# Kernel tuning notes

Hardware: AMD Instinct MI355X
Metric: run time of the kernel (lower is better)

## Reference

```python
import jax, jax.numpy as jnp
import numpy as np

T, B, D_IN, D_LAT, D_OUT = 2048, 64, 256, 256, 256


def _linear_params(key, fan_in, fan_out):
    kw, kb = jax.random.split(key)
    bound = 1.0 / np.sqrt(fan_in)
    W = jax.random.uniform(kw, (fan_out, fan_in), jnp.float32, -bound, bound)
    b = jax.random.uniform(kb, (fan_out,), jnp.float32, -bound, bound)
    return W, b


def setup_inputs() -> dict:
    key = jax.random.key(0)
    ks = jax.random.split(key, 6)
    Wf, bf = _linear_params(ks[0], D_IN + D_LAT, D_LAT)
    Wi, bi = _linear_params(ks[1], D_IN + D_LAT, D_LAT)
    Wo, bo = _linear_params(ks[2], D_IN + D_LAT, D_LAT)
    Wc, bc = _linear_params(ks[3], D_IN + D_LAT, D_LAT)
    Wout, bout = _linear_params(ks[4], D_LAT, D_OUT)
    x = jax.random.normal(ks[5], (T, B, D_IN), jnp.float32)
    h0 = jnp.zeros((B, D_LAT), jnp.float32)
    C0 = jnp.zeros((B, D_LAT), jnp.float32)
    return {"x": x, "h0": h0, "C0": C0,
            "Wf": Wf, "bf": bf, "Wi": Wi, "bi": bi,
            "Wo": Wo, "bo": bo, "Wc": Wc, "bc": bc,
            "Wout": Wout, "bout": bout}


def reference(x, h0, C0, Wf, bf, Wi, bi, Wo, bo, Wc, bc, Wout, bout):
    def step(carry, x_t):
        h, C = carry
        comb = jnp.concatenate([x_t, h], axis=-1)  # [B, D_IN+D_LAT]
        f_t = jax.nn.sigmoid(comb @ Wf.T + bf)
        i_t = jax.nn.sigmoid(comb @ Wi.T + bi)
        o_t = jax.nn.sigmoid(comb @ Wo.T + bo)
        C_tilde = jnp.tanh(comb @ Wc.T + bc)
        C_new = f_t * C + i_t * C_tilde
        h_new = o_t * jnp.tanh(C_new)
        out = h_new @ Wout.T + bout
        return (h_new, C_new), (out, h_new)
    (h_f, C_f), (outputs, hidden_states) = jax.lax.scan(step, (h0, C0), x)
    return outputs, hidden_states, C_f
```

## Files before the change

### kernel.cpp

```cpp
#include <hip/hip_runtime.h>
#include <cstdint>
#include <cstddef>

#define T_STEPS 2048
#define BATCH 64

typedef _Float16 f16;
typedef _Float16 f16x2 __attribute__((ext_vector_type(2)));
typedef _Float16 f16x8 __attribute__((ext_vector_type(8)));
typedef float f32x4 __attribute__((ext_vector_type(4)));
typedef unsigned int uint32;
typedef unsigned long long uint64;
typedef uint32 u32x4 __attribute__((ext_vector_type(4)));

__device__ __forceinline__ float dot2(uint32 w, uint32 h, float c) {
  f16x2 a = __builtin_bit_cast(f16x2, w);
  f16x2 b = __builtin_bit_cast(f16x2, h);
  return __builtin_amdgcn_fdot2(a, b, c, false);
}

__device__ __forceinline__ float dot8(u32x4 w, u32x4 h, float c) {
  c = dot2(w[0], h[0], c);
  c = dot2(w[1], h[1], c);
  c = dot2(w[2], h[2], c);
  c = dot2(w[3], h[3], c);
  return c;
}

__device__ __forceinline__ uint32 pack2(f16 a, f16 b) {
  f16x2 t; t[0] = a; t[1] = b;
  return __builtin_bit_cast(uint32, t);
}

__global__ __launch_bounds__(256) void setup_weights(
    const float* __restrict__ Wf, const float* __restrict__ Wi,
    const float* __restrict__ Wo, const float* __restrict__ Wc,
    const float* __restrict__ Wout,
    f16* __restrict__ wx16, f16* __restrict__ wout16, uint32* __restrict__ whp)
{
  int id = blockIdx.x * 256 + threadIdx.x;
  const float* WG_[4] = {Wf, Wi, Wo, Wc};
  if (id < 262144) {
    int n = id >> 8, k = id & 255;
    int G = n >> 8, j = n & 255;
    wx16[id] = (f16)WG_[G][j * 512 + k];
    return;
  }
  id -= 262144;
  if (id < 65536) { wout16[id] = (f16)Wout[id]; return; }
  id -= 65536;
  if (id < 131072) {
    int kq = id >> 12, rem = id & 4095;
    int o = rem >> 2, c = rem & 3;
    int G = o >> 8, j = o & 255;
    const float* src = WG_[G] + j * 512 + 256 + kq * 8 + c * 2;
    whp[id] = pack2((f16)src[0], (f16)src[1]);
  }
}

__global__ __launch_bounds__(256) void setup_state(
    const float* __restrict__ h0, const float* __restrict__ C0,
    uint64* __restrict__ hpair, float* __restrict__ c32)
{
  int id = blockIdx.x * 256 + threadIdx.x;
  if (id < 8192) {
    int slot = id >> 6, i = id & 63;
    int r = slot >> 1, hf = slot & 1;
    const float* hr = h0 + r * 256 + hf * 128 + 2 * i;
    uint32 a = (uint32)__builtin_bit_cast(unsigned short, (f16)hr[0]);
    uint32 b = (uint32)__builtin_bit_cast(unsigned short, (f16)hr[1]);
    hpair[id] = ((uint64)b << 32) | (uint64)a;
    return;
  }
  id -= 8192;
  if (id < 8192) { hpair[8192 + id] = 0xFFFF0000FFFF0000ULL; return; }
  id -= 8192;
  if (id < 16384) c32[id] = C0[id];
}

template<int A_F32, int OUT_F32_BIAS>
__global__ __launch_bounds__(256) void gemm_k(
    const void* __restrict__ Av, const f16* __restrict__ B,
    void* __restrict__ Cv, const float* __restrict__ bias, int N)
{
  constexpr int LDA = 264;
  __shared__ f16 As[128 * 264];
  __shared__ f16 Bs[128 * 264];
  const int tid = threadIdx.x;
  const int m0 = blockIdx.x * 128;
  const int n0 = blockIdx.y * 128;

  if (A_F32) {
    const float* A = (const float*)Av;
    #pragma unroll
    for (int j = 0; j < 32; ++j) {
      int flat = (tid + j * 256) * 4;
      int row = flat >> 8, col = flat & 255;
      const float4 v = *(const float4*)(A + (size_t)(m0 + row) * 256 + col);
      uint2 u; u.x = pack2((f16)v.x, (f16)v.y); u.y = pack2((f16)v.z, (f16)v.w);
      *(uint2*)&As[row * LDA + col] = u;
    }
  } else {
    const f16* A = (const f16*)Av;
    #pragma unroll
    for (int j = 0; j < 32; ++j) {
      int flat = (tid + j * 256) * 4;
      int row = flat >> 8, col = flat & 255;
      *(uint2*)&As[row * LDA + col] = *(const uint2*)(A + (size_t)(m0 + row) * 256 + col);
    }
  }
  #pragma unroll
  for (int j = 0; j < 32; ++j) {
    int flat = (tid + j * 256) * 4;
    int row = flat >> 8, col = flat & 255;
    *(uint2*)&Bs[row * LDA + col] = *(const uint2*)(B + (size_t)(n0 + row) * 256 + col);
  }
  __syncthreads();

  const int wave = tid >> 6, l = tid & 63;
  const int wr = wave >> 1, wc = wave & 1;
  const int lr = l & 15, lq = l >> 4;

  f32x4 acc[4][4] = {};
  #pragma unroll
  for (int kk = 0; kk < 8; ++kk) {
    f16x8 a[4], b[4];
    #pragma unroll
    for (int mi = 0; mi < 4; ++mi)
      a[mi] = *(const f16x8*)&As[(64 * wr + 16 * mi + lr) * LDA + kk * 32 + lq * 8];
    #pragma unroll
    for (int ni = 0; ni < 4; ++ni)
      b[ni] = *(const f16x8*)&Bs[(64 * wc + 16 * ni + lr) * LDA + kk * 32 + lq * 8];
    #pragma unroll
    for (int mi = 0; mi < 4; ++mi)
      #pragma unroll
      for (int ni = 0; ni < 4; ++ni)
        acc[mi][ni] = __builtin_amdgcn_mfma_f32_16x16x32_f16(a[mi], b[ni], acc[mi][ni], 0, 0, 0);
  }

  #pragma unroll
  for (int mi = 0; mi < 4; ++mi) {
    #pragma unroll
    for (int ni = 0; ni < 4; ++ni) {
      int col = n0 + 64 * wc + 16 * ni + lr;
      float bv = 0.f;
      if (OUT_F32_BIAS) bv = bias[col];
      #pragma unroll
      for (int v = 0; v < 4; ++v) {
        int row = m0 + 64 * wr + 16 * mi + lq * 4 + v;
        if (OUT_F32_BIAS) ((float*)Cv)[(size_t)row * N + col] = acc[mi][ni][v] + bv;
        else              ((f16*)Cv)[(size_t)row * N + col] = (f16)acc[mi][ni][v];
      }
    }
  }
}

#define RLO16(M) M(0) M(1) M(2) M(3) M(4) M(5) M(6) M(7) M(8) M(9) M(10) M(11) \
  M(12) M(13) M(14) M(15)
#define RLS4(M) M(0) M(1) M(2) M(3)

__global__ __launch_bounds__(512) void lstm_persist(
    const uint32* __restrict__ whp,
    const float* __restrict__ bf, const float* __restrict__ bi,
    const float* __restrict__ bo, const float* __restrict__ bc,
    const f16* __restrict__ xproj, uint64* __restrict__ hpair,
    float* __restrict__ c32, float* __restrict__ hid_out,
    f16* __restrict__ h16c, float* __restrict__ cf_out, int t0, int Tc)
{
  __shared__ u32x4 wlds[12 * 512];
  __shared__ uint32 h_lds[128] __attribute__((aligned(16)));
  __shared__ float part[4 * 132];
  __shared__ unsigned short hstage[128];

  const int tid = threadIdx.x;
  const int w = blockIdx.x;
  const int hf  = (w >> 3) & 1;
  const int r   = (w & 7) | ((w >> 4) << 3);
  const int G = tid >> 7, jjl = tid & 127;
  const int j = hf * 128 + jjl;
  const int o = (G << 8) + j;

  const int hfo = hf * 64;
  const int sfo = (hf ^ 1) * 64;
  const int okq = hf * 16;
  const int skq = (hf ^ 1) * 16;

  const u32x4* wq = (const u32x4*)whp;

#define LOADO(i) u32x4 wo##i = wq[(okq + (i)) * 1024 + o];
  RLO16(LOADO)
#undef LOADO
#define LOADS(i) u32x4 ws##i = wq[(skq + (i)) * 1024 + o];
  RLS4(LOADS)
#undef LOADS
  #pragma unroll
  for (int i = 0; i < 12; ++i)
    wlds[i * 512 + tid] = wq[(skq + 4 + i) * 1024 + o];

  const float* bGp = (G == 0) ? bf : (G == 1) ? bi : (G == 2) ? bo : bc;
  const float biasv = bGp[j];

  float Creg = 0.f;
  if (tid < 128) Creg = c32[r * 256 + j];

  uint64* mybuf  = hpair + (size_t)(r * 2 + hf) * 64;
  uint64* sibbuf = hpair + (size_t)(r * 2 + (hf ^ 1)) * 64;

  for (int tl = 0; tl < Tc; ++tl) {
    const int gt = t0 + tl;
    const int pp = gt & 1;

    const float xpv = (float)xproj[((size_t)tl * 64 + r) * 1024 + o];

    if (tid < 64) {
      const uint64* p = sibbuf + (size_t)pp * 8192 + tid;
      const uint32 tg = (uint32)gt;
      uint64 v = __hip_atomic_load(p, __ATOMIC_RELAXED, __HIP_MEMORY_SCOPE_AGENT);
      int tries = 0;
      while (((((uint32)v) >> 16) != tg || ((uint32)(v >> 48)) != tg) &&
             ++tries < (1 << 22)) {
        v = __hip_atomic_load(p, __ATOMIC_RELAXED, __HIP_MEMORY_SCOPE_AGENT);
      }
      h_lds[sfo + tid] =
          (((uint32)v) & 0xFFFFu) | ((((uint32)(v >> 32)) & 0xFFFFu) << 16);
    } else if (tl == 0 && tid < 128) {
      const int i = tid - 64;
      const uint64* p = mybuf + (size_t)pp * 8192 + i;
      const uint32 tg = (uint32)gt;
      uint64 v = __hip_atomic_load(p, __ATOMIC_RELAXED, __HIP_MEMORY_SCOPE_AGENT);
      int tries = 0;
      while (((((uint32)v) >> 16) != tg || ((uint32)(v >> 48)) != tg) &&
             ++tries < (1 << 22)) {
        v = __hip_atomic_load(p, __ATOMIC_RELAXED, __HIP_MEMORY_SCOPE_AGENT);
      }
      h_lds[hfo + i] =
          (((uint32)v) & 0xFFFFu) | ((((uint32)(v >> 32)) & 0xFFFFu) << 16);
    }
    __syncthreads();

    int otid;
    asm volatile("v_mov_b32 %0, %1" : "=v"(otid) : "v"(tid));
    float acc = 0.f;
#define DOT_O(i) { const u32x4 hh = *(const u32x4*)&h_lds[hfo + (i) * 4]; \
                   acc = dot8(wo##i, hh, acc); }
    RLO16(DOT_O)
#undef DOT_O
#define DOT_S(i) { const u32x4 hh = *(const u32x4*)&h_lds[sfo + (i) * 4]; \
                   acc = dot8(ws##i, hh, acc); }
    RLS4(DOT_S)
#undef DOT_S
    #pragma unroll
    for (int i = 0; i < 12; ++i) {
      const u32x4 hh = *(const u32x4*)&h_lds[sfo + (4 + i) * 4];
      acc = dot8(wlds[i * 512 + otid], hh, acc);
    }
    part[G * 132 + jjl] = acc + xpv + biasv;
    __syncthreads();

    if (tid < 128) {
      const float pf = part[tid];
      const float pi = part[132 + tid];
      const float po = part[264 + tid];
      const float pc = part[396 + tid];
      const float f_ = __builtin_amdgcn_rcpf(1.f + __expf(-pf));
      const float i_ = __builtin_amdgcn_rcpf(1.f + __expf(-pi));
      const float o_ = __builtin_amdgcn_rcpf(1.f + __expf(-po));
      const float cb = 1.f - 2.f * __builtin_amdgcn_rcpf(__expf(2.f * pc) + 1.f);
      const float Cn = f_ * Creg + i_ * cb;
      Creg = Cn;
      const float th = 1.f - 2.f * __builtin_amdgcn_rcpf(__expf(2.f * Cn) + 1.f);
      const float hn = o_ * th;
      hid_out[((size_t)gt * 64 + r) * 256 + j] = hn;
      const f16 h16v = (f16)hn;
      hstage[tid] = __builtin_bit_cast(unsigned short, h16v);
      h16c[((size_t)tl * 64 + r) * 256 + j] = h16v;
      if (gt == T_STEPS - 1) cf_out[r * 256 + j] = Cn;
    }
    __syncthreads();

    if (tid < 64) {
      const uint32 a = (uint32)hstage[2 * tid];
      const uint32 b = (uint32)hstage[2 * tid + 1];
      h_lds[hfo + tid] = a | (b << 16);
      const uint32 tg1u = ((uint32)(gt + 1)) << 16;
      const uint64 v = ((uint64)(b | tg1u) << 32) | (uint64)(a | tg1u);
      __hip_atomic_store(mybuf + (size_t)((gt + 1) & 1) * 8192 + tid, v,
                         __ATOMIC_RELAXED, __HIP_MEMORY_SCOPE_AGENT);
    }
  }

  if (tid < 128) c32[r * 256 + j] = Creg;
}

extern "C" void kernel_launch(void* const* d_in, const int* in_sizes, int n_in,
                              void* d_out, int out_size, void* d_ws, size_t ws_size,
                              hipStream_t stream)
{
  const float* x    = (const float*)d_in[0];
  const float* h0   = (const float*)d_in[1];
  const float* C0   = (const float*)d_in[2];
  const float* Wf   = (const float*)d_in[3];
  const float* bf   = (const float*)d_in[4];
  const float* Wi   = (const float*)d_in[5];
  const float* bi   = (const float*)d_in[6];
  const float* Wo   = (const float*)d_in[7];
  const float* bo   = (const float*)d_in[8];
  const float* Wc   = (const float*)d_in[9];
  const float* bc   = (const float*)d_in[10];
  const float* Wout = (const float*)d_in[11];
  const float* bout = (const float*)d_in[12];
  float* out = (float*)d_out;

  char* w = (char*)d_ws;
  f16*    wx16   = (f16*)w;    w += (size_t)1024 * 256 * 2;
  f16*    wout16 = (f16*)w;    w += (size_t)256 * 256 * 2;
  uint32* whp    = (uint32*)w; w += (size_t)131072 * 4;
  uint64* hpair  = (uint64*)w; w += (size_t)2 * 8192 * 8;
  float*  c32    = (float*)w;  w += (size_t)64 * 256 * 4;
  const size_t fixedB = (size_t)(w - (char*)d_ws);

  int Tc = 2;
  const int cands[] = {2048, 1024, 512, 256, 128, 64, 32, 16, 8, 4, 2};
  for (int c : cands) {
    if (fixedB + (size_t)c * 163840 <= ws_size) { Tc = c; break; }
  }

  f16* xproj = (f16*)w;
  f16* h16c  = (f16*)(w + (size_t)Tc * 64 * 1024 * 2);

  setup_weights<<<1792, 256, 0, stream>>>(Wf, Wi, Wo, Wc, Wout,
                                          wx16, wout16, whp);
  setup_state<<<128, 256, 0, stream>>>(h0, C0, hpair, c32);

  float* hid_out = out + (size_t)T_STEPS * 64 * 256;
  float* cf_out  = out + (size_t)2 * T_STEPS * 64 * 256;

  for (int t0 = 0; t0 < T_STEPS; t0 += Tc) {
    gemm_k<1, 0><<<dim3(Tc * 64 / 128, 8), 256, 0, stream>>>(
        x + (size_t)t0 * 64 * 256, wx16, xproj, nullptr, 1024);
    lstm_persist<<<128, 512, 0, stream>>>(whp, bf, bi, bo, bc,
                                          xproj, hpair, c32,
                                          hid_out, h16c, cf_out, t0, Tc);
    gemm_k<0, 1><<<dim3(Tc * 64 / 128, 2), 256, 0, stream>>>(
        h16c, wout16, out + (size_t)t0 * 64 * 256, bout, 256);
  }
}
```

Measured before the change: 3.711 ms.

## Split each batch row's LSTM hidden units across four workgroups instead of two

New measurement: 3.813 ms. 1.03x slower.

```diff
diff --git a/kernel.cpp b/kernel.cpp
--- a/kernel.cpp
+++ b/kernel.cpp
@@ -60,20 +60,20 @@
 
 __global__ __launch_bounds__(256) void setup_state(
     const float* __restrict__ h0, const float* __restrict__ C0,
-    uint64* __restrict__ hpair, float* __restrict__ c32)
+    uint64* __restrict__ hbuf, float* __restrict__ c32)
 {
   int id = blockIdx.x * 256 + threadIdx.x;
   if (id < 8192) {
-    int slot = id >> 6, i = id & 63;
-    int r = slot >> 1, hf = slot & 1;
-    const float* hr = h0 + r * 256 + hf * 128 + 2 * i;
+    int slot = id >> 5, i = id & 31;
+    int r = slot >> 2, q = slot & 3;
+    const float* hr = h0 + r * 256 + q * 64 + 2 * i;
     uint32 a = (uint32)__builtin_bit_cast(unsigned short, (f16)hr[0]);
     uint32 b = (uint32)__builtin_bit_cast(unsigned short, (f16)hr[1]);
-    hpair[id] = ((uint64)b << 32) | (uint64)a;
+    hbuf[id] = ((uint64)b << 32) | (uint64)a;
     return;
   }
   id -= 8192;
-  if (id < 8192) { hpair[8192 + id] = 0xFFFF0000FFFF0000ULL; return; }
+  if (id < 8192) { hbuf[8192 + id] = 0xFFFF0000FFFF0000ULL; return; }
   id -= 8192;
   if (id < 16384) c32[id] = C0[id];
 }
@@ -155,56 +155,45 @@
   }
 }
 
-#define RLO16(M) M(0) M(1) M(2) M(3) M(4) M(5) M(6) M(7) M(8) M(9) M(10) M(11) \
-  M(12) M(13) M(14) M(15)
-#define RLS4(M) M(0) M(1) M(2) M(3)
-
-__global__ __launch_bounds__(512) void lstm_persist(
+#define RL20(M) M(0) M(1) M(2) M(3) M(4) M(5) M(6) M(7) M(8) M(9) M(10) M(11) \
+  M(12) M(13) M(14) M(15) M(16) M(17) M(18) M(19)
+
+__global__ __launch_bounds__(256) void lstm_persist(
     const uint32* __restrict__ whp,
     const float* __restrict__ bf, const float* __restrict__ bi,
     const float* __restrict__ bo, const float* __restrict__ bc,
-    const f16* __restrict__ xproj, uint64* __restrict__ hpair,
+    const f16* __restrict__ xproj, uint64* __restrict__ hbuf,
     float* __restrict__ c32, float* __restrict__ hid_out,
     f16* __restrict__ h16c, float* __restrict__ cf_out, int t0, int Tc)
 {
-  __shared__ u32x4 wlds[12 * 512];
+  __shared__ u32x4 wlds[12 * 256];
   __shared__ uint32 h_lds[128] __attribute__((aligned(16)));
-  __shared__ float part[4 * 132];
-  __shared__ unsigned short hstage[128];
+  __shared__ float part[4 * 68];
+  __shared__ unsigned short hstage[64];
 
   const int tid = threadIdx.x;
   const int w = blockIdx.x;
-  const int hf  = (w >> 3) & 1;
-  const int r   = (w & 7) | ((w >> 4) << 3);
-  const int G = tid >> 7, jjl = tid & 127;
-  const int j = hf * 128 + jjl;
+  const int q = w >> 6, r = w & 63;
+  const int G = tid >> 6, col = tid & 63;
+  const int j = q * 64 + col;
   const int o = (G << 8) + j;
 
-  const int hfo = hf * 64;
-  const int sfo = (hf ^ 1) * 64;
-  const int okq = hf * 16;
-  const int skq = (hf ^ 1) * 16;
-
   const u32x4* wq = (const u32x4*)whp;
 
-#define LOADO(i) u32x4 wo##i = wq[(okq + (i)) * 1024 + o];
-  RLO16(LOADO)
-#undef LOADO
-#define LOADS(i) u32x4 ws##i = wq[(skq + (i)) * 1024 + o];
-  RLS4(LOADS)
-#undef LOADS
+#define LOADW(i) u32x4 w##i = wq[(i) * 1024 + o];
+  RL20(LOADW)
+#undef LOADW
   #pragma unroll
   for (int i = 0; i < 12; ++i)
-    wlds[i * 512 + tid] = wq[(skq + 4 + i) * 1024 + o];
+    wlds[i * 256 + tid] = wq[(20 + i) * 1024 + o];
 
   const float* bGp = (G == 0) ? bf : (G == 1) ? bi : (G == 2) ? bo : bc;
   const float biasv = bGp[j];
 
   float Creg = 0.f;
-  if (tid < 128) Creg = c32[r * 256 + j];
-
-  uint64* mybuf  = hpair + (size_t)(r * 2 + hf) * 64;
-  uint64* sibbuf = hpair + (size_t)(r * 2 + (hf ^ 1)) * 64;
+  if (tid < 64) Creg = c32[r * 256 + q * 64 + tid];
+
+  uint64* mybuf = hbuf + (size_t)(r * 4 + q) * 32;
 
   for (int tl = 0; tl < Tc; ++tl) {
     const int gt = t0 + tl;
@@ -212,56 +201,54 @@
 
     const float xpv = (float)xproj[((size_t)tl * 64 + r) * 1024 + o];
 
-    if (tid < 64) {
-      const uint64* p = sibbuf + (size_t)pp * 8192 + tid;
+    if (tid < 96) {
+      const int s = tid >> 5, i = tid & 31;
+      const int qq = s + (s >= q ? 1 : 0);
+      const uint64* p = hbuf + (size_t)pp * 8192 + (size_t)(r * 4 + qq) * 32 + i;
       const uint32 tg = (uint32)gt;
       uint64 v = __hip_atomic_load(p, __ATOMIC_RELAXED, __HIP_MEMORY_SCOPE_AGENT);
       int tries = 0;
       while (((((uint32)v) >> 16) != tg || ((uint32)(v >> 48)) != tg) &&
-             ++tries < (1 << 22)) {
+             ++tries < (1 << 20)) {
         v = __hip_atomic_load(p, __ATOMIC_RELAXED, __HIP_MEMORY_SCOPE_AGENT);
       }
-      h_lds[sfo + tid] =
+      h_lds[qq * 32 + i] =
           (((uint32)v) & 0xFFFFu) | ((((uint32)(v >> 32)) & 0xFFFFu) << 16);
     } else if (tl == 0 && tid < 128) {
-      const int i = tid - 64;
+      const int i = tid - 96;
       const uint64* p = mybuf + (size_t)pp * 8192 + i;
       const uint32 tg = (uint32)gt;
       uint64 v = __hip_atomic_load(p, __ATOMIC_RELAXED, __HIP_MEMORY_SCOPE_AGENT);
       int tries = 0;
       while (((((uint32)v) >> 16) != tg || ((uint32)(v >> 48)) != tg) &&
-             ++tries < (1 << 22)) {
+             ++tries < (1 << 20)) {
         v = __hip_atomic_load(p, __ATOMIC_RELAXED, __HIP_MEMORY_SCOPE_AGENT);
       }
-      h_lds[hfo + i] =
+      h_lds[q * 32 + i] =
           (((uint32)v) & 0xFFFFu) | ((((uint32)(v >> 32)) & 0xFFFFu) << 16);
     }
     __syncthreads();
 
     int otid;
     asm volatile("v_mov_b32 %0, %1" : "=v"(otid) : "v"(tid));
-    float acc = 0.f;
-#define DOT_O(i) { const u32x4 hh = *(const u32x4*)&h_lds[hfo + (i) * 4]; \
-                   acc = dot8(wo##i, hh, acc); }
-    RLO16(DOT_O)
-#undef DOT_O
-#define DOT_S(i) { const u32x4 hh = *(const u32x4*)&h_lds[sfo + (i) * 4]; \
-                   acc = dot8(ws##i, hh, acc); }
-    RLS4(DOT_S)
-#undef DOT_S
+    float ac[4] = {0.f, 0.f, 0.f, 0.f};
+#define DOTW(i) { const u32x4 hh = *(const u32x4*)&h_lds[(i) * 4]; \
+                  ac[(i) & 3] = dot8(w##i, hh, ac[(i) & 3]); }
+    RL20(DOTW)
+#undef DOTW
     #pragma unroll
     for (int i = 0; i < 12; ++i) {
-      const u32x4 hh = *(const u32x4*)&h_lds[sfo + (4 + i) * 4];
-      acc = dot8(wlds[i * 512 + otid], hh, acc);
-    }
-    part[G * 132 + jjl] = acc + xpv + biasv;
+      const u32x4 hh = *(const u32x4*)&h_lds[(20 + i) * 4];
+      ac[(20 + i) & 3] = dot8(wlds[i * 256 + otid], hh, ac[(20 + i) & 3]);
+    }
+    part[G * 68 + col] = (ac[0] + ac[1]) + (ac[2] + ac[3]) + xpv + biasv;
     __syncthreads();
 
-    if (tid < 128) {
+    if (tid < 64) {
       const float pf = part[tid];
-      const float pi = part[132 + tid];
-      const float po = part[264 + tid];
-      const float pc = part[396 + tid];
+      const float pi = part[68 + tid];
+      const float po = part[136 + tid];
+      const float pc = part[204 + tid];
       const float f_ = __builtin_amdgcn_rcpf(1.f + __expf(-pf));
       const float i_ = __builtin_amdgcn_rcpf(1.f + __expf(-pi));
       const float o_ = __builtin_amdgcn_rcpf(1.f + __expf(-po));
@@ -270,18 +257,19 @@
       Creg = Cn;
       const float th = 1.f - 2.f * __builtin_amdgcn_rcpf(__expf(2.f * Cn) + 1.f);
       const float hn = o_ * th;
-      hid_out[((size_t)gt * 64 + r) * 256 + j] = hn;
+      const int jg = q * 64 + tid;
+      hid_out[((size_t)gt * 64 + r) * 256 + jg] = hn;
       const f16 h16v = (f16)hn;
       hstage[tid] = __builtin_bit_cast(unsigned short, h16v);
-      h16c[((size_t)tl * 64 + r) * 256 + j] = h16v;
-      if (gt == T_STEPS - 1) cf_out[r * 256 + j] = Cn;
+      h16c[((size_t)tl * 64 + r) * 256 + jg] = h16v;
+      if (gt == T_STEPS - 1) cf_out[r * 256 + jg] = Cn;
     }
     __syncthreads();
 
-    if (tid < 64) {
+    if (tid < 32) {
       const uint32 a = (uint32)hstage[2 * tid];
       const uint32 b = (uint32)hstage[2 * tid + 1];
-      h_lds[hfo + tid] = a | (b << 16);
+      h_lds[q * 32 + tid] = a | (b << 16);
       const uint32 tg1u = ((uint32)(gt + 1)) << 16;
       const uint64 v = ((uint64)(b | tg1u) << 32) | (uint64)(a | tg1u);
       __hip_atomic_store(mybuf + (size_t)((gt + 1) & 1) * 8192 + tid, v,
@@ -289,7 +277,7 @@
     }
   }
 
-  if (tid < 128) c32[r * 256 + j] = Creg;
+  if (tid < 64) c32[r * 256 + q * 64 + tid] = Creg;
 }
 
 extern "C" void kernel_launch(void* const* d_in, const int* in_sizes, int n_in,
@@ -315,7 +303,7 @@
   f16*    wx16   = (f16*)w;    w += (size_t)1024 * 256 * 2;
   f16*    wout16 = (f16*)w;    w += (size_t)256 * 256 * 2;
   uint32* whp    = (uint32*)w; w += (size_t)131072 * 4;
-  uint64* hpair  = (uint64*)w; w += (size_t)2 * 8192 * 8;
+  uint64* hbuf   = (uint64*)w; w += (size_t)2 * 8192 * 8;
   float*  c32    = (float*)w;  w += (size_t)64 * 256 * 4;
   const size_t fixedB = (size_t)(w - (char*)d_ws);
 
@@ -330,7 +318,7 @@
 
   setup_weights<<<1792, 256, 0, stream>>>(Wf, Wi, Wo, Wc, Wout,
                                           wx16, wout16, whp);
-  setup_state<<<128, 256, 0, stream>>>(h0, C0, hpair, c32);
+  setup_state<<<128, 256, 0, stream>>>(h0, C0, hbuf, c32);
 
   float* hid_out = out + (size_t)T_STEPS * 64 * 256;
   float* cf_out  = out + (size_t)2 * T_STEPS * 64 * 256;
@@ -338,8 +326,8 @@
   for (int t0 = 0; t0 < T_STEPS; t0 += Tc) {
     gemm_k<1, 0><<<dim3(Tc * 64 / 128, 8), 256, 0, stream>>>(
         x + (size_t)t0 * 64 * 256, wx16, xproj, nullptr, 1024);
-    lstm_persist<<<128, 512, 0, stream>>>(whp, bf, bi, bo, bc,
-                                          xproj, hpair, c32,
+    lstm_persist<<<256, 256, 0, stream>>>(whp, bf, bi, bo, bc,
+                                          xproj, hbuf, c32,
                                           hid_out, h16c, cf_out, t0, Tc);
     gemm_k<0, 1><<<dim3(Tc * 64 / 128, 2), 256, 0, stream>>>(
         h16c, wout16, out + (size_t)t0 * 64 * 256, bout, 256);
```

## Gather LSTM gates with wave shuffles and overlap own-half dot with sibling wait

Applied to the files above, without the earlier changes.

Measured after the change: 3.376 ms. 1.1x faster.

```diff
diff --git a/kernel.cpp b/kernel.cpp
--- a/kernel.cpp
+++ b/kernel.cpp
@@ -60,7 +60,7 @@
 
 __global__ __launch_bounds__(256) void setup_state(
     const float* __restrict__ h0, const float* __restrict__ C0,
-    uint64* __restrict__ hpair, float* __restrict__ c32)
+    uint64* __restrict__ hbuf, float* __restrict__ c32)
 {
   int id = blockIdx.x * 256 + threadIdx.x;
   if (id < 8192) {
@@ -69,11 +69,11 @@
     const float* hr = h0 + r * 256 + hf * 128 + 2 * i;
     uint32 a = (uint32)__builtin_bit_cast(unsigned short, (f16)hr[0]);
     uint32 b = (uint32)__builtin_bit_cast(unsigned short, (f16)hr[1]);
-    hpair[id] = ((uint64)b << 32) | (uint64)a;
+    hbuf[id] = ((uint64)b << 32) | (uint64)a;
     return;
   }
   id -= 8192;
-  if (id < 8192) { hpair[8192 + id] = 0xFFFF0000FFFF0000ULL; return; }
+  if (id < 8192) { hbuf[8192 + id] = 0xFFFF0000FFFF0000ULL; return; }
   id -= 8192;
   if (id < 16384) c32[id] = C0[id];
 }
@@ -163,22 +163,21 @@
     const uint32* __restrict__ whp,
     const float* __restrict__ bf, const float* __restrict__ bi,
     const float* __restrict__ bo, const float* __restrict__ bc,
-    const f16* __restrict__ xproj, uint64* __restrict__ hpair,
+    const f16* __restrict__ xproj, uint64* __restrict__ hbuf,
     float* __restrict__ c32, float* __restrict__ hid_out,
     f16* __restrict__ h16c, float* __restrict__ cf_out, int t0, int Tc)
 {
   __shared__ u32x4 wlds[12 * 512];
   __shared__ uint32 h_lds[128] __attribute__((aligned(16)));
-  __shared__ float part[4 * 132];
-  __shared__ unsigned short hstage[128];
 
   const int tid = threadIdx.x;
   const int w = blockIdx.x;
   const int hf  = (w >> 3) & 1;
   const int r   = (w & 7) | ((w >> 4) << 3);
-  const int G = tid >> 7, jjl = tid & 127;
-  const int j = hf * 128 + jjl;
-  const int o = (G << 8) + j;
+  const int wv = tid >> 6, l = tid & 63;
+  const int g = l >> 4, cl = l & 15;
+  const int j = hf * 128 + 16 * wv + cl;
+  const int o = (g << 8) + j;
 
   const int hfo = hf * 64;
   const int sfo = (hf ^ 1) * 64;
@@ -197,20 +196,41 @@
   for (int i = 0; i < 12; ++i)
     wlds[i * 512 + tid] = wq[(skq + 4 + i) * 1024 + o];
 
-  const float* bGp = (G == 0) ? bf : (G == 1) ? bi : (G == 2) ? bo : bc;
+  const float* bGp = (g == 0) ? bf : (g == 1) ? bi : (g == 2) ? bo : bc;
   const float biasv = bGp[j];
 
-  float Creg = 0.f;
-  if (tid < 128) Creg = c32[r * 256 + j];
-
-  uint64* mybuf  = hpair + (size_t)(r * 2 + hf) * 64;
-  uint64* sibbuf = hpair + (size_t)(r * 2 + (hf ^ 1)) * 64;
+  float Creg = c32[r * 256 + j];
+
+  uint64* mybuf  = hbuf + (size_t)(r * 2 + hf) * 64;
+  uint64* sibbuf = hbuf + (size_t)(r * 2 + (hf ^ 1)) * 64;
+
+  if (tid < 64) {
+    const uint64* p = mybuf + (size_t)(t0 & 1) * 8192 + tid;
+    const uint32 tg = (uint32)t0;
+    uint64 v = __hip_atomic_load(p, __ATOMIC_RELAXED, __HIP_MEMORY_SCOPE_AGENT);
+    int tries = 0;
+    while (((((uint32)v) >> 16) != tg || ((uint32)(v >> 48)) != tg) &&
+           ++tries < (1 << 22)) {
+      v = __hip_atomic_load(p, __ATOMIC_RELAXED, __HIP_MEMORY_SCOPE_AGENT);
+    }
+    h_lds[hfo + tid] =
+        (((uint32)v) & 0xFFFFu) | ((((uint32)(v >> 32)) & 0xFFFFu) << 16);
+  }
+  __syncthreads();
 
   for (int tl = 0; tl < Tc; ++tl) {
     const int gt = t0 + tl;
     const int pp = gt & 1;
 
     const float xpv = (float)xproj[((size_t)tl * 64 + r) * 1024 + o];
+
+    float ac0 = 0.f, ac1 = 0.f, ac2 = 0.f, ac3 = 0.f;
+#define DOT_O(i) { const u32x4 hh = *(const u32x4*)&h_lds[hfo + (i) * 4]; \
+                   float& A_ = (((i) & 3) == 0) ? ac0 : (((i) & 3) == 1) ? ac1 \
+                             : (((i) & 3) == 2) ? ac2 : ac3; \
+                   A_ = dot8(wo##i, hh, A_); }
+    RLO16(DOT_O)
+#undef DOT_O
 
     if (tid < 64) {
       const uint64* p = sibbuf + (size_t)pp * 8192 + tid;
@@ -223,73 +243,65 @@
       }
       h_lds[sfo + tid] =
           (((uint32)v) & 0xFFFFu) | ((((uint32)(v >> 32)) & 0xFFFFu) << 16);
-    } else if (tl == 0 && tid < 128) {
-      const int i = tid - 64;
-      const uint64* p = mybuf + (size_t)pp * 8192 + i;
-      const uint32 tg = (uint32)gt;
-      uint64 v = __hip_atomic_load(p, __ATOMIC_RELAXED, __HIP_MEMORY_SCOPE_AGENT);
-      int tries = 0;
-      while (((((uint32)v) >> 16) != tg || ((uint32)(v >> 48)) != tg) &&
-             ++tries < (1 << 22)) {
-        v = __hip_atomic_load(p, __ATOMIC_RELAXED, __HIP_MEMORY_SCOPE_AGENT);
-      }
-      h_lds[hfo + i] =
-          (((uint32)v) & 0xFFFFu) | ((((uint32)(v >> 32)) & 0xFFFFu) << 16);
     }
     __syncthreads();
 
     int otid;
     asm volatile("v_mov_b32 %0, %1" : "=v"(otid) : "v"(tid));
-    float acc = 0.f;
-#define DOT_O(i) { const u32x4 hh = *(const u32x4*)&h_lds[hfo + (i) * 4]; \
-                   acc = dot8(wo##i, hh, acc); }
-    RLO16(DOT_O)
-#undef DOT_O
 #define DOT_S(i) { const u32x4 hh = *(const u32x4*)&h_lds[sfo + (i) * 4]; \
-                   acc = dot8(ws##i, hh, acc); }
+                   float& A_ = (((i) & 3) == 0) ? ac0 : (((i) & 3) == 1) ? ac1 \
+                             : (((i) & 3) == 2) ? ac2 : ac3; \
+                   A_ = dot8(ws##i, hh, A_); }
     RLS4(DOT_S)
 #undef DOT_S
     #pragma unroll
     for (int i = 0; i < 12; ++i) {
       const u32x4 hh = *(const u32x4*)&h_lds[sfo + (4 + i) * 4];
-      acc = dot8(wlds[i * 512 + otid], hh, acc);
-    }
-    part[G * 132 + jjl] = acc + xpv + biasv;
-    __syncthreads();
-
-    if (tid < 128) {
-      const float pf = part[tid];
-      const float pi = part[132 + tid];
-      const float po = part[264 + tid];
-      const float pc = part[396 + tid];
-      const float f_ = __builtin_amdgcn_rcpf(1.f + __expf(-pf));
-      const float i_ = __builtin_amdgcn_rcpf(1.f + __expf(-pi));
-      const float o_ = __builtin_amdgcn_rcpf(1.f + __expf(-po));
-      const float cb = 1.f - 2.f * __builtin_amdgcn_rcpf(__expf(2.f * pc) + 1.f);
-      const float Cn = f_ * Creg + i_ * cb;
-      Creg = Cn;
-      const float th = 1.f - 2.f * __builtin_amdgcn_rcpf(__expf(2.f * Cn) + 1.f);
-      const float hn = o_ * th;
+      float& A_ = (((4 + i) & 3) == 0) ? ac0 : (((4 + i) & 3) == 1) ? ac1
+                : (((4 + i) & 3) == 2) ? ac2 : ac3;
+      A_ = dot8(wlds[i * 512 + otid], hh, A_);
+    }
+    const float acc = (ac0 + ac1) + (ac2 + ac3) + xpv + biasv;
+
+    const float a  = acc;
+    const float b  = __shfl_xor(acc, 16, 64);
+    const float cx = __shfl_xor(acc, 32, 64);
+    const float d  = __shfl_xor(b, 32, 64);
+    const float pf = (g == 0) ? a  : (g == 1) ? b  : (g == 2) ? cx : d;
+    const float pi = (g == 0) ? b  : (g == 1) ? a  : (g == 2) ? d  : cx;
+    const float po = (g == 0) ? cx : (g == 1) ? d  : (g == 2) ? a  : b;
+    const float pc = (g == 0) ? d  : (g == 1) ? cx : (g == 2) ? b  : a;
+
+    const float f_ = __builtin_amdgcn_rcpf(1.f + __expf(-pf));
+    const float i_ = __builtin_amdgcn_rcpf(1.f + __expf(-pi));
+    const float o_ = __builtin_amdgcn_rcpf(1.f + __expf(-po));
+    const float cb = 1.f - 2.f * __builtin_amdgcn_rcpf(__expf(2.f * pc) + 1.f);
+    const float Cn = f_ * Creg + i_ * cb;
+    Creg = Cn;
+    const float th = 1.f - 2.f * __builtin_amdgcn_rcpf(__expf(2.f * Cn) + 1.f);
+    const float hn = o_ * th;
+    const f16 h16v = (f16)hn;
+
+    if (g == 0) {
       hid_out[((size_t)gt * 64 + r) * 256 + j] = hn;
-      const f16 h16v = (f16)hn;
-      hstage[tid] = __builtin_bit_cast(unsigned short, h16v);
       h16c[((size_t)tl * 64 + r) * 256 + j] = h16v;
       if (gt == T_STEPS - 1) cf_out[r * 256 + j] = Cn;
     }
+
+    const uint32 hb = (uint32)__builtin_bit_cast(unsigned short, h16v);
+    const uint32 nb = __shfl_xor((int)hb, 1, 64);
+    if (g == 0 && (cl & 1) == 0) {
+      const int m = 8 * wv + (cl >> 1);
+      h_lds[hfo + m] = hb | (nb << 16);
+      const uint32 tg1u = ((uint32)(gt + 1)) << 16;
+      const uint64 v = ((uint64)(nb | tg1u) << 32) | (uint64)(hb | tg1u);
+      __hip_atomic_store(mybuf + (size_t)((gt + 1) & 1) * 8192 + m, v,
+                         __ATOMIC_RELAXED, __HIP_MEMORY_SCOPE_AGENT);
+    }
     __syncthreads();
-
-    if (tid < 64) {
-      const uint32 a = (uint32)hstage[2 * tid];
-      const uint32 b = (uint32)hstage[2 * tid + 1];
-      h_lds[hfo + tid] = a | (b << 16);
-      const uint32 tg1u = ((uint32)(gt + 1)) << 16;
-      const uint64 v = ((uint64)(b | tg1u) << 32) | (uint64)(a | tg1u);
-      __hip_atomic_store(mybuf + (size_t)((gt + 1) & 1) * 8192 + tid, v,
-                         __ATOMIC_RELAXED, __HIP_MEMORY_SCOPE_AGENT);
-    }
-  }
-
-  if (tid < 128) c32[r * 256 + j] = Creg;
+  }
+
+  if (g == 0) c32[r * 256 + j] = Creg;
 }
 
 extern "C" void kernel_launch(void* const* d_in, const int* in_sizes, int n_in,
@@ -315,7 +327,7 @@
   f16*    wx16   = (f16*)w;    w += (size_t)1024 * 256 * 2;
   f16*    wout16 = (f16*)w;    w += (size_t)256 * 256 * 2;
   uint32* whp    = (uint32*)w; w += (size_t)131072 * 4;
-  uint64* hpair  = (uint64*)w; w += (size_t)2 * 8192 * 8;
+  uint64* hbuf   = (uint64*)w; w += (size_t)2 * 8192 * 8;
   float*  c32    = (float*)w;  w += (size_t)64 * 256 * 4;
   const size_t fixedB = (size_t)(w - (char*)d_ws);
 
@@ -330,7 +342,7 @@
 
   setup_weights<<<1792, 256, 0, stream>>>(Wf, Wi, Wo, Wc, Wout,
                                           wx16, wout16, whp);
-  setup_state<<<128, 256, 0, stream>>>(h0, C0, hpair, c32);
+  setup_state<<<128, 256, 0, stream>>>(h0, C0, hbuf, c32);
 
   float* hid_out = out + (size_t)T_STEPS * 64 * 256;
   float* cf_out  = out + (size_t)2 * T_STEPS * 64 * 256;
@@ -339,7 +351,7 @@
     gemm_k<1, 0><<<dim3(Tc * 64 / 128, 8), 256, 0, stream>>>(
         x + (size_t)t0 * 64 * 256, wx16, xproj, nullptr, 1024);
     lstm_persist<<<128, 512, 0, stream>>>(whp, bf, bi, bo, bc,
-                                          xproj, hpair, c32,
+                                          xproj, hbuf, c32,
                                           hid_out, h16c, cf_out, t0, Tc);
     gemm_k<0, 1><<<dim3(Tc * 64 / 128, 2), 256, 0, stream>>>(
         h16c, wout16, out + (size_t)t0 * 64 * 256, bout, 256);
```
